# Optimization experiments

Hardware: AMD Instinct MI355X
Metric: run time of the kernel (lower is better)

The kernel has to match this reference:

```python
import jax, jax.numpy as jnp
import numpy as np

N_ENT = 50000
N_REL = 500
N_EDGE = 640000
D_IN = 128
D_OUT = 128
NEG_SLOPE = 0.01  # torch nn.LeakyReLU default
BN_EPS = 1e-5


def setup_inputs() -> dict:
    key = jax.random.key(0)
    ks = jax.random.split(key, 16)
    edge_index = jax.random.randint(ks[0], (2, N_EDGE), 0, N_ENT)
    edge_type = jax.random.randint(ks[1], (N_EDGE,), 0, N_REL)
    query_type = jax.random.randint(ks[2], (N_EDGE,), 0, N_REL)
    entity_embed = jax.random.normal(ks[3], (N_ENT, D_IN), jnp.float32)
    rel_embed = jax.random.normal(ks[4], (N_REL, D_IN), jnp.float32)
    s = 0.05
    return {
        "edge_index": edge_index,
        "edge_type": edge_type,
        "query_type": query_type,
        "entity_embed": entity_embed,
        "rel_embed": rel_embed,
        "w_loop": jax.random.normal(ks[5], (D_IN, D_OUT), jnp.float32) * s,
        "w_out": jax.random.normal(ks[6], (D_IN, D_OUT), jnp.float32) * s,
        "w_rel": jax.random.normal(ks[7], (D_IN, D_OUT), jnp.float32) * s,
        "loop_rel": jax.random.normal(ks[8], (1, D_IN), jnp.float32) * s,
        "W_w": jax.random.normal(ks[9], (D_IN, D_IN), jnp.float32) * s,   # W.weight^T layout: x @ W_w
        "W_b": jnp.zeros((D_IN,), jnp.float32),
        "a_w": jax.random.normal(ks[10], (2 * D_IN, 1), jnp.float32) * s,
        "a_b": jnp.zeros((1,), jnp.float32),
        "bias": jnp.zeros((D_OUT,), jnp.float32),
        "bn_gamma": jnp.ones((D_OUT,), jnp.float32),
        "bn_beta": jnp.zeros((D_OUT,), jnp.float32),
    }


def _compgcn_fwd(edge_index, edge_type, query_type, entity_embed, rel_embed,
                 w_loop, w_out, w_rel, loop_rel, W_w, W_b, a_w, a_b,
                 bias, bn_gamma, bn_beta):
    N = entity_embed.shape[0]
    rel_all = jnp.concatenate([rel_embed, loop_rel], axis=0)  # (R+1, D)
    row, col = edge_index[0], edge_index[1]  # values already in [0, N)

    # edge norm: 1/out-degree of source node (deg[row] >= 1 for every edge)
    deg = jax.ops.segment_sum(jnp.ones((row.shape[0],), entity_embed.dtype), row, num_segments=N)
    norm = 1.0 / deg[row]  # (E,)

    # self-loop branch (mode='loop'): rel_transform 'mult' with loop relation, no attention
    loop_res = (entity_embed * rel_all[-1]) @ w_loop  # (N, D_out)

    # out branch (mode='out')
    x_j = entity_embed[col]          # (E, D)
    r_e = rel_all[edge_type]         # (E, D)
    q_e = rel_all[query_type]        # (E, D)
    xj_rel = x_j * r_e               # 'mult' composition

    h = jnp.concatenate([r_e @ W_w + W_b, q_e @ W_w + W_b], axis=-1)  # (E, 2D)
    logits = h @ a_w + a_b                                            # (E, 1)
    alpha = jnp.exp(jax.nn.leaky_relu(logits[:, 0], NEG_SLOPE))       # (E,)
    sum_alpha = jax.ops.segment_sum(alpha, row, num_segments=N)       # (N,)
    alpha = alpha / sum_alpha[row]

    msg = (xj_rel @ w_out) * (alpha * norm)[:, None]                  # (E, D_out)
    out_res = jax.ops.segment_sum(msg, row, num_segments=N)           # (N, D_out)

    out = 0.5 * out_res + 0.5 * loop_res + bias  # dropout = identity (eval)
    # BatchNorm1d, training-mode batch statistics (biased var), over node dim
    mean = jnp.mean(out, axis=0)
    var = jnp.mean((out - mean) ** 2, axis=0)
    out = (out - mean) * jax.lax.rsqrt(var + BN_EPS) * bn_gamma + bn_beta

    ent_out = jax.nn.leaky_relu(out, NEG_SLOPE)
    rel_out = (rel_all @ w_rel)[:-1]
    return ent_out, rel_out


def reference(edge_index, edge_type, query_type, entity_embed, rel_embed,
              w_loop, w_out, w_rel, loop_rel, W_w, W_b, a_w, a_b,
              bias, bn_gamma, bn_beta):
    return _compgcn_fwd(edge_index, edge_type, query_type, entity_embed, rel_embed,
                        w_loop, w_out, w_rel, loop_rel, W_w, W_b, a_w, a_b,
                        bias, bn_gamma, bn_beta)
```

## Files before the change

kernel.cpp:

```cpp
#include <hip/hip_runtime.h>
#include <math.h>

#define E_N 640000
#define N_N 50000
#define R_N 500
#define D   128
#define NEG 0.01f
#define BNEPS 1e-5f
#define CAP 48

typedef __bf16 bf16x8 __attribute__((ext_vector_type(8)));
typedef float f32x4 __attribute__((ext_vector_type(4)));

#define CNT_OFF    0u
#define STAT_OFF   50000u
#define ZERO_FLOATS 50256u
#define BUCKET_OFF 50256u
#define STAGE_OFF  4850256u
#define BT_OFF     11256400u
#define S1_OFF     11272784u
#define S2_OFF     11273296u

__device__ __forceinline__ float lrelu(float x) { return x > 0.f ? x : NEG * x; }

__device__ __forceinline__ void st_bf16x4(__bf16* p, float x, float y, float z, float w) {
    union { __bf16 b[4]; uint2 u; } pk;
    pk.b[0] = (__bf16)x; pk.b[1] = (__bf16)y; pk.b[2] = (__bf16)z; pk.b[3] = (__bf16)w;
    *(uint2*)p = pk.u;
}

#define PREP_S   501
#define PREP_WB  256
#define PREP_REL 500

__global__ __launch_bounds__(128) void k_prep(const float* __restrict__ Ww,
                                              const float* __restrict__ Wb,
                                              const float* __restrict__ aw,
                                              const float* __restrict__ rel,
                                              const float* __restrict__ looprel,
                                              const float* __restrict__ wout,
                                              const float* __restrict__ wloop,
                                              const float* __restrict__ wrel,
                                              float* __restrict__ s1,
                                              float* __restrict__ s2,
                                              __bf16* __restrict__ Bt,
                                              float* __restrict__ out_rel) {
    int b = blockIdx.x, t = threadIdx.x;
    if (b < PREP_S) {
        __shared__ float rr[D];
        __shared__ float part[4];
        const float* rp = (b < R_N) ? rel + (size_t)b * D : looprel;
        rr[t] = rp[t];
        __syncthreads();
        float v = 0.f;
        for (int i = 0; i < D; ++i) v = fmaf(rr[i], Ww[i * D + t], v);
        float p1 = aw[t] * v + Wb[t] * aw[t];
        float p2 = aw[D + t] * v + Wb[t] * aw[D + t];
        for (int o = 32; o; o >>= 1) {
            p1 += __shfl_down(p1, o);
            p2 += __shfl_down(p2, o);
        }
        if ((t & 63) == 0) {
            part[(t >> 6) * 2] = p1;
            part[(t >> 6) * 2 + 1] = p2;
        }
        __syncthreads();
        if (t == 0) {
            s1[b] = part[0] + part[2];
            s2[b] = part[1] + part[3];
        }
    } else if (b < PREP_S + PREP_WB) {
        int idx = (b - PREP_S) * 128 + t;
        int n = idx & 127, k = idx >> 7;
        float v = (k < D) ? wout[(size_t)k * D + n] : wloop[(size_t)(k - D) * D + n];
        Bt[(size_t)n * 256 + k] = (__bf16)v;
    } else {
        int r = b - (PREP_S + PREP_WB);
        __shared__ float rr2[D];
        rr2[t] = rel[(size_t)r * D + t];
        __syncthreads();
        float a = 0.f;
        for (int k = 0; k < D; ++k) a = fmaf(rr2[k], wrel[(size_t)k * D + t], a);
        out_rel[(size_t)r * D + t] = a;
    }
}

__global__ __launch_bounds__(256) void k_bin(const int* __restrict__ row,
                                             const int* __restrict__ col,
                                             const int* __restrict__ et,
                                             const int* __restrict__ qt,
                                             int* __restrict__ cnt,
                                             int2* __restrict__ bucket) {
    int e = blockIdx.x * blockDim.x + threadIdx.x;
    if (e >= E_N) return;
    int r = row[e];
    int pos = atomicAdd(&cnt[r], 1);
    if (pos < CAP) {
        bucket[(size_t)r * CAP + pos] = make_int2(col[e], et[e] | (qt[e] << 16));
    }
}

__global__ __launch_bounds__(128) void k_gather(const int* __restrict__ cnt,
                                                const int2* __restrict__ bucket,
                                                const float* __restrict__ s1,
                                                const float* __restrict__ s2,
                                                const float* __restrict__ ab,
                                                const float* __restrict__ ent,
                                                const float* __restrict__ rel,
                                                const float* __restrict__ looprel,
                                                __bf16* __restrict__ stage) {
    int n = blockIdx.x, t = threadIdx.x;
    int deg = cnt[n];
    int m = deg < CAP ? deg : CAP;
    __shared__ int eoff[CAP];
    __shared__ int roff[CAP];
    __shared__ float sa[CAP];
    __shared__ float xred[32][4];
    if (t < m) {
        int2 be = bucket[(size_t)n * CAP + t];
        eoff[t] = be.x << 9;
        int e_t = be.y & 0xffff;
        int q_t = be.y >> 16;
        roff[t] = e_t << 9;
        sa[t] = expf(lrelu(s1[e_t] + s2[q_t] + ab[0]));
    }
    __syncthreads();
    float suma = 0.f;
    for (int i = 0; i < m; ++i) suma += sa[i];
    int s = t & 31, g = t >> 5;
    const char* entb = (const char*)ent;
    const char* relb = (const char*)rel;
    int co = s * 16;
    float ax = 0.f, ay = 0.f, az = 0.f, aw4 = 0.f;
    float bx = 0.f, by = 0.f, bz = 0.f, bw = 0.f;
    for (int i = 0; i < m; i += 8) {
        int e0 = i + g, e1 = i + g + 4;
        if (e0 < m) {
            float4 ev = *(const float4*)(entb + (eoff[e0] + co));
            float4 rv = *(const float4*)(relb + (roff[e0] + co));
            float a = sa[e0];
            ax = fmaf(a * ev.x, rv.x, ax);
            ay = fmaf(a * ev.y, rv.y, ay);
            az = fmaf(a * ev.z, rv.z, az);
            aw4 = fmaf(a * ev.w, rv.w, aw4);
        }
        if (e1 < m) {
            float4 ev = *(const float4*)(entb + (eoff[e1] + co));
            float4 rv = *(const float4*)(relb + (roff[e1] + co));
            float a = sa[e1];
            bx = fmaf(a * ev.x, rv.x, bx);
            by = fmaf(a * ev.y, rv.y, by);
            bz = fmaf(a * ev.z, rv.z, bz);
            bw = fmaf(a * ev.w, rv.w, bw);
        }
    }
    ax += bx; ay += by; az += bz; aw4 += bw;
    ax += __shfl_xor(ax, 32);
    ay += __shfl_xor(ay, 32);
    az += __shfl_xor(az, 32);
    aw4 += __shfl_xor(aw4, 32);
    if (t >= 64 && t < 96) {
        xred[s][0] = ax; xred[s][1] = ay; xred[s][2] = az; xred[s][3] = aw4;
    }
    if (t >= 32 && t < 64) {
        int s2i = t - 32;
        float4 e4 = *(const float4*)(entb + ((size_t)n << 9) + s2i * 16);
        float4 l4 = ((const float4*)looprel)[s2i];
        st_bf16x4(stage + (size_t)n * 256 + 128 + s2i * 4,
                  e4.x * l4.x, e4.y * l4.y, e4.z * l4.z, e4.w * l4.w);
    }
    __syncthreads();
    if (t < 32) {
        float inv = (deg > 0) ? 1.0f / (suma * (float)deg) : 0.f;
        st_bf16x4(stage + (size_t)n * 256 + s * 4,
                  (ax + xred[s][0]) * inv, (ay + xred[s][1]) * inv,
                  (az + xred[s][2]) * inv, (aw4 + xred[s][3]) * inv);
    }
}

__global__ __launch_bounds__(256) void k_gemm(const __bf16* __restrict__ stage,
                                              const __bf16* __restrict__ Bt,
                                              const float* __restrict__ bias,
                                              float* __restrict__ out,
                                              float* __restrict__ stat) {
    int t = threadIdx.x;
    int wave = t >> 6, l = t & 63;
    int lm = l & 15, lg = l >> 4;
    size_t mbase = (size_t)blockIdx.x * 128 + wave * 32;
    const bf16x8* A = (const bf16x8*)stage;
    const bf16x8* B = (const bf16x8*)Bt;
    f32x4 acc[2][8];
#pragma unroll
    for (int mt = 0; mt < 2; ++mt)
#pragma unroll
        for (int nt = 0; nt < 8; ++nt) acc[mt][nt] = (f32x4)(0.f);
#pragma unroll
    for (int ks = 0; ks < 8; ++ks) {
        bf16x8 a0 = A[(mbase + lm) * 32 + ks * 4 + lg];
        bf16x8 a1 = A[(mbase + 16 + lm) * 32 + ks * 4 + lg];
#pragma unroll
        for (int nt = 0; nt < 8; ++nt) {
            bf16x8 b = B[(size_t)(nt * 16 + lm) * 32 + ks * 4 + lg];
            acc[0][nt] = __builtin_amdgcn_mfma_f32_16x16x32_bf16(a0, b, acc[0][nt], 0, 0, 0);
            acc[1][nt] = __builtin_amdgcn_mfma_f32_16x16x32_bf16(a1, b, acc[1][nt], 0, 0, 0);
        }
    }
    float psum[8], psq[8];
#pragma unroll
    for (int nt = 0; nt < 8; ++nt) { psum[nt] = 0.f; psq[nt] = 0.f; }
#pragma unroll
    for (int mt = 0; mt < 2; ++mt) {
#pragma unroll
        for (int nt = 0; nt < 8; ++nt) {
            int c = nt * 16 + lm;
            float bv = bias[c];
#pragma unroll
            for (int r = 0; r < 4; ++r) {
                size_t rowi = mbase + mt * 16 + lg * 4 + r;
                if (rowi < N_N) {
                    float v = 0.5f * acc[mt][nt][r] + bv;
                    out[rowi * D + c] = v;
                    psum[nt] += v;
                    psq[nt] += v * v;
                }
            }
        }
    }
    __shared__ float2 red[8][16][16];
    int slot = wave * 4 + lg;
#pragma unroll
    for (int nt = 0; nt < 8; ++nt) red[nt][lm][slot] = make_float2(psum[nt], psq[nt]);
    __syncthreads();
    if (t < 128) {
        int nt = t >> 4, lmm = t & 15;
        float ss = 0.f, qq = 0.f;
#pragma unroll
        for (int k = 0; k < 16; ++k) {
            float2 v = red[nt][lmm][k];
            ss += v.x;
            qq += v.y;
        }
        atomicAdd(&stat[t], ss);
        atomicAdd(&stat[D + t], qq);
    }
}

__global__ __launch_bounds__(256) void k_bnapply(float* __restrict__ out,
                                                 const float* __restrict__ stat,
                                                 const float* __restrict__ gamma,
                                                 const float* __restrict__ beta) {
    __shared__ float ssc[D], ssh[D];
    int t = threadIdx.x;
    if (t < D) {
        float mean = stat[t] * (1.0f / N_N);
        float var = stat[D + t] * (1.0f / N_N) - mean * mean;
        float sc = gamma[t] * rsqrtf(var + BNEPS);
        ssc[t] = sc;
        ssh[t] = beta[t] - mean * sc;
    }
    __syncthreads();
    const float4* sc4 = (const float4*)ssc;
    const float4* sh4 = (const float4*)ssh;
    float4* o4 = (float4*)out;
    const int total = N_N * D / 4;
    for (int i = blockIdx.x * blockDim.x + t; i < total; i += gridDim.x * blockDim.x) {
        int d4 = i & 31;
        float4 v = o4[i];
        float4 s = sc4[d4];
        float4 h = sh4[d4];
        v.x = lrelu(v.x * s.x + h.x);
        v.y = lrelu(v.y * s.y + h.y);
        v.z = lrelu(v.z * s.z + h.z);
        v.w = lrelu(v.w * s.w + h.w);
        o4[i] = v;
    }
}

extern "C" void kernel_launch(void* const* d_in, const int* in_sizes, int n_in,
                              void* d_out, int out_size, void* d_ws, size_t ws_size,
                              hipStream_t stream) {
    const int* edge_index = (const int*)d_in[0];
    const int* row = edge_index;
    const int* col = edge_index + E_N;
    const int* etype = (const int*)d_in[1];
    const int* qtype = (const int*)d_in[2];
    const float* ent = (const float*)d_in[3];
    const float* rel = (const float*)d_in[4];
    const float* w_loop = (const float*)d_in[5];
    const float* w_out = (const float*)d_in[6];
    const float* w_rel = (const float*)d_in[7];
    const float* loop_rel = (const float*)d_in[8];
    const float* W_w = (const float*)d_in[9];
    const float* W_b = (const float*)d_in[10];
    const float* a_w = (const float*)d_in[11];
    const float* a_b = (const float*)d_in[12];
    const float* bias = (const float*)d_in[13];
    const float* bn_gamma = (const float*)d_in[14];
    const float* bn_beta = (const float*)d_in[15];

    float* ws = (float*)d_ws;
    int* cnt = (int*)(ws + CNT_OFF);
    float* stat = ws + STAT_OFF;
    int2* bucket = (int2*)(ws + BUCKET_OFF);
    __bf16* stage = (__bf16*)(ws + STAGE_OFF);
    __bf16* Bt = (__bf16*)(ws + BT_OFF);
    float* s1 = ws + S1_OFF;
    float* s2 = ws + S2_OFF;

    float* out_ent = (float*)d_out;
    float* out_rel = out_ent + (size_t)N_N * D;

    hipMemsetAsync(d_ws, 0, (size_t)ZERO_FLOATS * sizeof(float), stream);
    hipMemsetAsync(stage + (size_t)N_N * 256, 0, (size_t)48 * 256 * sizeof(__bf16),
                   stream);

    k_prep<<<PREP_S + PREP_WB + PREP_REL, 128, 0, stream>>>(
        W_w, W_b, a_w, rel, loop_rel, w_out, w_loop, w_rel, s1, s2, Bt, out_rel);
    k_bin<<<(E_N + 255) / 256, 256, 0, stream>>>(row, col, etype, qtype, cnt, bucket);
    k_gather<<<N_N, 128, 0, stream>>>(cnt, bucket, s1, s2, a_b, ent, rel, loop_rel,
                                      stage);
    k_gemm<<<(N_N + 127) / 128, 256, 0, stream>>>(stage, Bt, bias, out_ent, stat);
    k_bnapply<<<2048, 256, 0, stream>>>(out_ent, stat, bn_gamma, bn_beta);
}
```

Baseline: 154.1 us.

## Pre-convert embeddings to bf16 for the gather and stage into the output buffer

The prep kernel gains extra blocks that convert the entity and relation embedding tables to bf16 once. The per-node gather kernel then reads half as many bytes per random neighbour row, unpacking bf16 pairs into fp32 FMAs with 16 lanes per row instead of 32. The staging buffer for the GEMM now lives in the output allocation, which saves workspace and one memset; the GEMM reads its own rows before overwriting them in place. The trade-offs are an extra full pass over the entity table, an extra bf16 rounding of the inputs before the multiply, and reliance on the in-place aliasing being safe, including padded rows past N.

```diff
diff --git a/kernel.cpp b/kernel.cpp
--- a/kernel.cpp
+++ b/kernel.cpp
@@ -16,10 +16,11 @@
 #define STAT_OFF   50000u
 #define ZERO_FLOATS 50256u
 #define BUCKET_OFF 50256u
-#define STAGE_OFF  4850256u
-#define BT_OFF     11256400u
-#define S1_OFF     11272784u
-#define S2_OFF     11273296u
+#define ENTBF_OFF  4850256u
+#define RELBF_OFF  8050256u
+#define BT_OFF     8082256u
+#define S1_OFF     8098640u
+#define S2_OFF     8099152u
 
 __device__ __forceinline__ float lrelu(float x) { return x > 0.f ? x : NEG * x; }
 
@@ -29,9 +30,31 @@
     *(uint2*)p = pk.u;
 }
 
+__device__ __forceinline__ void st_bf16x8(__bf16* p, const float* v) {
+    union { __bf16 b[8]; uint4 u; } pk;
+#pragma unroll
+    for (int j = 0; j < 8; ++j) pk.b[j] = (__bf16)v[j];
+    *(uint4*)p = pk.u;
+}
+
+__device__ __forceinline__ void fma8(uint4 ue, uint4 ur, float a, float* acc) {
+    const unsigned* we = (const unsigned*)&ue;
+    const unsigned* wr = (const unsigned*)&ur;
+#pragma unroll
+    for (int w = 0; w < 4; ++w) {
+        float e_lo = __uint_as_float(we[w] << 16);
+        float e_hi = __uint_as_float(we[w] & 0xffff0000u);
+        float r_lo = __uint_as_float(wr[w] << 16);
+        float r_hi = __uint_as_float(wr[w] & 0xffff0000u);
+        acc[2 * w]     = fmaf(a * e_lo, r_lo, acc[2 * w]);
+        acc[2 * w + 1] = fmaf(a * e_hi, r_hi, acc[2 * w + 1]);
+    }
+}
+
 #define PREP_S   501
 #define PREP_WB  256
 #define PREP_REL 500
+#define PREP_ENT 3125
 
 __global__ __launch_bounds__(128) void k_prep(const float* __restrict__ Ww,
                                               const float* __restrict__ Wb,
@@ -41,16 +64,20 @@
                                               const float* __restrict__ wout,
                                               const float* __restrict__ wloop,
                                               const float* __restrict__ wrel,
+                                              const float* __restrict__ ent,
                                               float* __restrict__ s1,
                                               float* __restrict__ s2,
                                               __bf16* __restrict__ Bt,
-                                              float* __restrict__ out_rel) {
+                                              float* __restrict__ out_rel,
+                                              __bf16* __restrict__ ent_bf,
+                                              __bf16* __restrict__ rel_bf) {
     int b = blockIdx.x, t = threadIdx.x;
     if (b < PREP_S) {
         __shared__ float rr[D];
         __shared__ float part[4];
         const float* rp = (b < R_N) ? rel + (size_t)b * D : looprel;
         rr[t] = rp[t];
+        if (b < R_N) rel_bf[(size_t)b * D + t] = (__bf16)rp[t];
         __syncthreads();
         float v = 0.f;
         for (int i = 0; i < D; ++i) v = fmaf(rr[i], Ww[i * D + t], v);
@@ -74,7 +101,7 @@
         int n = idx & 127, k = idx >> 7;
         float v = (k < D) ? wout[(size_t)k * D + n] : wloop[(size_t)(k - D) * D + n];
         Bt[(size_t)n * 256 + k] = (__bf16)v;
-    } else {
+    } else if (b < PREP_S + PREP_WB + PREP_REL) {
         int r = b - (PREP_S + PREP_WB);
         __shared__ float rr2[D];
         rr2[t] = rel[(size_t)r * D + t];
@@ -82,6 +109,15 @@
         float a = 0.f;
         for (int k = 0; k < D; ++k) a = fmaf(rr2[k], wrel[(size_t)k * D + t], a);
         out_rel[(size_t)r * D + t] = a;
+    } else {
+        int blk = b - (PREP_S + PREP_WB + PREP_REL);
+        const float4* e4 = (const float4*)ent;
+#pragma unroll
+        for (int j = 0; j < 4; ++j) {
+            int idx = blk * 512 + j * 128 + t;
+            float4 v = e4[idx];
+            st_bf16x4(ent_bf + (size_t)idx * 4, v.x, v.y, v.z, v.w);
+        }
     }
 }
 
@@ -105,8 +141,8 @@
                                                 const float* __restrict__ s1,
                                                 const float* __restrict__ s2,
                                                 const float* __restrict__ ab,
-                                                const float* __restrict__ ent,
-                                                const float* __restrict__ rel,
+                                                const __bf16* __restrict__ ent_bf,
+                                                const __bf16* __restrict__ rel_bf,
                                                 const float* __restrict__ looprel,
                                                 __bf16* __restrict__ stage) {
     int n = blockIdx.x, t = threadIdx.x;
@@ -115,73 +151,73 @@
     __shared__ int eoff[CAP];
     __shared__ int roff[CAP];
     __shared__ float sa[CAP];
-    __shared__ float xred[32][4];
+    __shared__ float xred[16][8];
     if (t < m) {
         int2 be = bucket[(size_t)n * CAP + t];
-        eoff[t] = be.x << 9;
+        eoff[t] = be.x << 8;
         int e_t = be.y & 0xffff;
         int q_t = be.y >> 16;
-        roff[t] = e_t << 9;
+        roff[t] = e_t << 8;
         sa[t] = expf(lrelu(s1[e_t] + s2[q_t] + ab[0]));
     }
     __syncthreads();
     float suma = 0.f;
     for (int i = 0; i < m; ++i) suma += sa[i];
-    int s = t & 31, g = t >> 5;
-    const char* entb = (const char*)ent;
-    const char* relb = (const char*)rel;
+    int s = t & 15, g = t >> 4;
+    const char* eb = (const char*)ent_bf;
+    const char* rb = (const char*)rel_bf;
     int co = s * 16;
-    float ax = 0.f, ay = 0.f, az = 0.f, aw4 = 0.f;
-    float bx = 0.f, by = 0.f, bz = 0.f, bw = 0.f;
-    for (int i = 0; i < m; i += 8) {
-        int e0 = i + g, e1 = i + g + 4;
+    float acc[8] = {0, 0, 0, 0, 0, 0, 0, 0};
+    float acc2[8] = {0, 0, 0, 0, 0, 0, 0, 0};
+    for (int i = 0; i < m; i += 16) {
+        int e0 = i + g, e1 = i + g + 8;
         if (e0 < m) {
-            float4 ev = *(const float4*)(entb + (eoff[e0] + co));
-            float4 rv = *(const float4*)(relb + (roff[e0] + co));
-            float a = sa[e0];
-            ax = fmaf(a * ev.x, rv.x, ax);
-            ay = fmaf(a * ev.y, rv.y, ay);
-            az = fmaf(a * ev.z, rv.z, az);
-            aw4 = fmaf(a * ev.w, rv.w, aw4);
+            uint4 ue = *(const uint4*)(eb + (eoff[e0] + co));
+            uint4 ur = *(const uint4*)(rb + (roff[e0] + co));
+            fma8(ue, ur, sa[e0], acc);
         }
         if (e1 < m) {
-            float4 ev = *(const float4*)(entb + (eoff[e1] + co));
-            float4 rv = *(const float4*)(relb + (roff[e1] + co));
-            float a = sa[e1];
-            bx = fmaf(a * ev.x, rv.x, bx);
-            by = fmaf(a * ev.y, rv.y, by);
-            bz = fmaf(a * ev.z, rv.z, bz);
-            bw = fmaf(a * ev.w, rv.w, bw);
-        }
-    }
-    ax += bx; ay += by; az += bz; aw4 += bw;
-    ax += __shfl_xor(ax, 32);
-    ay += __shfl_xor(ay, 32);
-    az += __shfl_xor(az, 32);
-    aw4 += __shfl_xor(aw4, 32);
-    if (t >= 64 && t < 96) {
-        xred[s][0] = ax; xred[s][1] = ay; xred[s][2] = az; xred[s][3] = aw4;
-    }
-    if (t >= 32 && t < 64) {
-        int s2i = t - 32;
-        float4 e4 = *(const float4*)(entb + ((size_t)n << 9) + s2i * 16);
-        float4 l4 = ((const float4*)looprel)[s2i];
-        st_bf16x4(stage + (size_t)n * 256 + 128 + s2i * 4,
-                  e4.x * l4.x, e4.y * l4.y, e4.z * l4.z, e4.w * l4.w);
+            uint4 ue = *(const uint4*)(eb + (eoff[e1] + co));
+            uint4 ur = *(const uint4*)(rb + (roff[e1] + co));
+            fma8(ue, ur, sa[e1], acc2);
+        }
+    }
+#pragma unroll
+    for (int k = 0; k < 8; ++k) {
+        acc[k] += acc2[k];
+        acc[k] += __shfl_xor(acc[k], 16);
+        acc[k] += __shfl_xor(acc[k], 32);
+    }
+    if (t >= 64 && t < 80) {
+#pragma unroll
+        for (int k = 0; k < 8; ++k) xred[s][k] = acc[k];
+    }
+    if (t >= 96 && t < 112) {
+        int si = t - 96;
+        uint4 ue = *(const uint4*)(eb + ((size_t)n << 8) + si * 16);
+        const unsigned* we = (const unsigned*)&ue;
+        float v[8];
+#pragma unroll
+        for (int w = 0; w < 4; ++w) {
+            v[2 * w]     = __uint_as_float(we[w] << 16) * looprel[si * 8 + 2 * w];
+            v[2 * w + 1] = __uint_as_float(we[w] & 0xffff0000u) * looprel[si * 8 + 2 * w + 1];
+        }
+        st_bf16x8(stage + (size_t)n * 256 + 128 + si * 8, v);
     }
     __syncthreads();
-    if (t < 32) {
+    if (t < 16) {
         float inv = (deg > 0) ? 1.0f / (suma * (float)deg) : 0.f;
-        st_bf16x4(stage + (size_t)n * 256 + s * 4,
-                  (ax + xred[s][0]) * inv, (ay + xred[s][1]) * inv,
-                  (az + xred[s][2]) * inv, (aw4 + xred[s][3]) * inv);
-    }
-}
-
-__global__ __launch_bounds__(256) void k_gemm(const __bf16* __restrict__ stage,
+        float v[8];
+#pragma unroll
+        for (int k = 0; k < 8; ++k) v[k] = (acc[k] + xred[s][k]) * inv;
+        st_bf16x8(stage + (size_t)n * 256 + s * 8, v);
+    }
+}
+
+__global__ __launch_bounds__(256) void k_gemm(const __bf16* stage,
                                               const __bf16* __restrict__ Bt,
                                               const float* __restrict__ bias,
-                                              float* __restrict__ out,
+                                              float* out,
                                               float* __restrict__ stat) {
     int t = threadIdx.x;
     int wave = t >> 6, l = t & 63;
@@ -302,23 +338,24 @@
     int* cnt = (int*)(ws + CNT_OFF);
     float* stat = ws + STAT_OFF;
     int2* bucket = (int2*)(ws + BUCKET_OFF);
-    __bf16* stage = (__bf16*)(ws + STAGE_OFF);
+    __bf16* ent_bf = (__bf16*)(ws + ENTBF_OFF);
+    __bf16* rel_bf = (__bf16*)(ws + RELBF_OFF);
     __bf16* Bt = (__bf16*)(ws + BT_OFF);
     float* s1 = ws + S1_OFF;
     float* s2 = ws + S2_OFF;
 
     float* out_ent = (float*)d_out;
     float* out_rel = out_ent + (size_t)N_N * D;
+    __bf16* stage = (__bf16*)d_out;
 
     hipMemsetAsync(d_ws, 0, (size_t)ZERO_FLOATS * sizeof(float), stream);
-    hipMemsetAsync(stage + (size_t)N_N * 256, 0, (size_t)48 * 256 * sizeof(__bf16),
-                   stream);
-
-    k_prep<<<PREP_S + PREP_WB + PREP_REL, 128, 0, stream>>>(
-        W_w, W_b, a_w, rel, loop_rel, w_out, w_loop, w_rel, s1, s2, Bt, out_rel);
+
+    k_prep<<<PREP_S + PREP_WB + PREP_REL + PREP_ENT, 128, 0, stream>>>(
+        W_w, W_b, a_w, rel, loop_rel, w_out, w_loop, w_rel, ent,
+        s1, s2, Bt, out_rel, ent_bf, rel_bf);
     k_bin<<<(E_N + 255) / 256, 256, 0, stream>>>(row, col, etype, qtype, cnt, bucket);
-    k_gather<<<N_N, 128, 0, stream>>>(cnt, bucket, s1, s2, a_b, ent, rel, loop_rel,
-                                      stage);
+    k_gather<<<N_N, 128, 0, stream>>>(cnt, bucket, s1, s2, a_b, ent_bf, rel_bf,
+                                      loop_rel, stage);
     k_gemm<<<(N_N + 127) / 128, 256, 0, stream>>>(stage, Bt, bias, out_ent, stat);
     k_bnapply<<<2048, 256, 0, stream>>>(out_ent, stat, bn_gamma, bn_beta);
 }
```

Result: faster. 146.3 us (-5.0%).
